# Optimization experiments

Hardware: AMD Instinct MI355X
Metric: run time of the kernel (lower is better)

Reference implementation:

```python
import jax, jax.numpy as jnp
import numpy as np

B, D, C, H = 4096, 64, 16, 512   # batch, state dim, conditional dim, MLP hidden
NBIJ, NSTEPS = 2, 8              # stacked FFJORD bijectors, fixed RK4 steps over t in [0,1]


def setup_inputs() -> dict:
    key = jax.random.key(0)
    ks = jax.random.split(key, 8)
    g = lambda k, shape, scale: (jax.random.normal(k, shape, jnp.float32) * scale).astype(jnp.float32)
    return {
        "x": jax.random.normal(ks[0], (B, D), jnp.float32),
        "cond": jax.random.normal(ks[1], (B, C), jnp.float32),
        "eps": jax.random.normal(ks[2], (NBIJ, B, D), jnp.float32),  # Hutchinson probes, one per bijector
        "W1": g(ks[3], (NBIJ, D + C + 1, H), (D + C + 1) ** -0.5),
        "b1": jnp.zeros((NBIJ, H), jnp.float32),
        "W2": g(ks[4], (NBIJ, H, H), H ** -0.5),
        "b2": jnp.zeros((NBIJ, H), jnp.float32),
        "W3": g(ks[5], (NBIJ, H, D), H ** -0.5),
        "b3": jnp.zeros((NBIJ, D), jnp.float32),
    }


def _mlp(t, y, cond, W1, b1, W2, b2, W3, b3):
    # state_time_derivative_fn(t, x, conditional_input=cond) -> [B, D]
    tcol = jnp.full((y.shape[0], 1), t, y.dtype)
    h = jnp.tanh(jnp.concatenate([y, cond, tcol], axis=-1) @ W1 + b1)
    h = jnp.tanh(h @ W2 + b2)
    return h @ W3 + b3


def _integrate(x, cond, eps, params):
    # Augmented ODE: dy/dt = f(t,y), d(logdet)/dt = tr(df/dy) ~= eps^T J eps (Hutchinson)
    dt = jnp.float32(1.0 / NSTEPS)

    def aug(t, y):
        f = lambda z: _mlp(t, z, cond, *params)
        out, vjp_fn = jax.vjp(f, y)
        (epsJ,) = vjp_fn(eps)
        return out, jnp.sum(epsJ * eps, axis=-1)

    def step(carry, i):
        y, ld = carry
        t = i * dt
        k1, l1 = aug(t, y)
        k2, l2 = aug(t + 0.5 * dt, y + (0.5 * dt) * k1)
        k3, l3 = aug(t + 0.5 * dt, y + (0.5 * dt) * k2)
        k4, l4 = aug(t + dt, y + dt * k3)
        y = y + (dt / 6.0) * (k1 + 2.0 * k2 + 2.0 * k3 + k4)
        ld = ld + (dt / 6.0) * (l1 + 2.0 * l2 + 2.0 * l3 + l4)
        return (y, ld), None

    ld0 = jnp.zeros((x.shape[0],), x.dtype)
    (y, ld), _ = jax.lax.scan(step, (x, ld0), jnp.arange(NSTEPS, dtype=x.dtype))
    return y, ld


def reference(x, cond, eps, W1, b1, W2, b2, W3, b3):
    # Chain forward: bijector0 then bijector1 (tfb.Chain(reversed(...)) applies in build order)
    y = x
    ld = jnp.zeros((x.shape[0],), x.dtype)
    for ib in range(NBIJ):
        params = (W1[ib], b1[ib], W2[ib], b2[ib], W3[ib], b3[ib])
        y, d = _integrate(y, cond, eps[ib], params)
        ld = ld + d
    # augmented output: transformed state + accumulated log|det J|
    return jnp.concatenate([y, ld[:, None]], axis=-1)
```

## Files before the change

### kernel.cpp

```cpp
#include <hip/hip_runtime.h>


typedef __attribute__((ext_vector_type(8))) short short8;
typedef __attribute__((ext_vector_type(4))) float f32x4;
typedef __attribute__((ext_vector_type(4))) int int4v;

#define MFMA_B16(a, b, c) __builtin_amdgcn_mfma_f32_16x16x32_bf16((a), (b), (c), 0, 0, 0)
#define MFMA_I8(a, b, c)  __builtin_amdgcn_mfma_i32_16x16x64_i8((a), (b), (c), 0, 0, 0)

__device__ __forceinline__ unsigned short f2bf(float f) {
  union { float f; unsigned u; } v; v.f = f;
  return (unsigned short)((v.u + 0x7FFFu + ((v.u >> 16) & 1u)) >> 16);
}
__device__ __forceinline__ float bf2f(unsigned short u) {
  union { unsigned u; float f; } v; v.u = ((unsigned)u) << 16; return v.f;
}
__device__ __forceinline__ float fast_tanh(float x) {
  float e = __expf(2.f * x);
  return 1.f - 2.f * __builtin_amdgcn_rcpf(e + 1.f);
}


__global__ void prep_scales(const float* __restrict__ W2, float* __restrict__ sc) {
  int idx = blockIdx.x * 256 + threadIdx.x;
  if (idx >= 1024) return;
  int ib = idx >> 9, n = idx & 511;
  const float* W = W2 + (size_t)ib * 262144;
  float m = 0.f;
  for (int k = 0; k < 512; ++k) m = fmaxf(m, fabsf(W[(size_t)k * 512 + n]));
  sc[idx] = fmaxf(m, 1e-8f);
}

__global__ void prep_bf16(const float* __restrict__ W1, const float* __restrict__ W2,
                          const float* __restrict__ W3, unsigned short* __restrict__ ws) {
  int o = blockIdx.x * 256 + threadIdx.x;
  char* ws8 = (char*)ws;
  const float* sc = (const float*)(ws8 + 1114112);
  if (o < 98304) {
    int ib = o / 49152, r = o % 49152, n = r / 96, k = r % 96;
    ws[o] = (k < 81) ? f2bf(W1[(size_t)ib * 41472 + k * 512 + n]) : (unsigned short)0;
  } else if (o < 622592) {
    int b = o - 98304;
    int ib = b / 262144, b2 = b % 262144;
    int p = b2 / 32768, r2 = b2 % 32768, n = r2 / 64, kk = r2 & 63;
    int k = p * 64 + (kk ^ (((n >> 1) & 3) << 4));
    float w = W2[(size_t)ib * 262144 + (size_t)k * 512 + n];
    float s = sc[ib * 512 + n];
    int q = (int)rintf(w * (127.f / s));
    q = q > 127 ? 127 : (q < -127 ? -127 : q);
    ws8[196608 + b] = (char)q;
  } else if (o < 688128) {
    int o2 = o - 622592;
    int ib = o2 / 32768, r = o2 % 32768, n = r / 512, k = r % 512;
    ws[360448 + o2] = f2bf(W3[(size_t)ib * 32768 + k * 64 + n]);
  } else if (o < 753664) {
    int o2 = o - 688128;
    ws[425984 + o2] = f2bf(W3[o2]);
  } else if (o < 819200) {
    int o2 = o - 753664;
    int ib = o2 / 32768, r = o2 % 32768, h = r / 64, d = r % 64;
    ws[491520 + o2] = f2bf(W1[(size_t)ib * 41472 + d * 512 + h]);
  }
}

#define ZS 104
#define HS 520
#define H8 528
#define INV2 (1.f / 16129.f)

#define ISSUE_STAGE(WP, KS, BUF) do {                                                   \
    const char* _s = (WP) + (KS) * 32768 + (wave << 11) + (lane << 4);                  \
    char* _d = &Bst[(BUF)][wave << 11];                                                 \
    __builtin_amdgcn_global_load_lds(                                                   \
        (const __attribute__((address_space(1))) void*)_s,                              \
        (__attribute__((address_space(3))) void*)_d, 16, 0, 0);                         \
    __builtin_amdgcn_global_load_lds(                                                   \
        (const __attribute__((address_space(1))) void*)(_s + 1024),                     \
        (__attribute__((address_space(3))) void*)(_d + 1024), 16, 0, 0);                \
  } while (0)

__global__ __launch_bounds__(1024) void ffjord_mfma(
    const float* __restrict__ x, const float* __restrict__ cond, const float* __restrict__ eps,
    const float* __restrict__ b1g, const float* __restrict__ b2g, const float* __restrict__ b3g,
    const unsigned short* __restrict__ ws, float* __restrict__ out) {
  __shared__ unsigned short zA[16 * ZS];
  __shared__ __align__(16) char h1A8[16 * H8];
  __shared__ __align__(16) char vA8[16 * H8];
  __shared__ unsigned short h2A[16 * HS];
  __shared__ __align__(16) char Bst[3][32768];
  __shared__ float f_s[16][64];
  __shared__ float l_row[16], ld_row[16], ldacc[16];
  __shared__ int sgu[16];

  const int t = threadIdx.x;
  const int wave = t >> 6;
  const int lane = t & 63;
  const int lane15 = lane & 15;
  const int q8 = (lane >> 4) * 8;
  const int q16 = (lane >> 4) * 16;
  const int rowb = q8 >> 1;
  const int row0 = blockIdx.x * 16;
  const int ws32 = wave * 32;
  const int nt3 = wave & 3;
  const int kb3 = (wave >> 2) * 128;
  const int tm = t >> 6, td = t & 63;

  const int kk2b = q16 ^ (((lane15 >> 1) & 3) << 4);

  float ycur, ytmp, yacc = 0.f;
  {
    float xv = x[(size_t)(row0 + tm) * 64 + td];
    ycur = xv; ytmp = xv;
  }
  if (t < 512) {
    int m = t >> 5, kk = t & 31;
    zA[m * ZS + 64 + kk] = (kk < 16) ? f2bf(cond[(size_t)(row0 + m) * 16 + kk]) : (unsigned short)0;
  }
  if (t < 16) { ld_row[t] = 0.f; l_row[t] = 0.f; }

  const float dt = 0.125f;
  const float w06 = dt / 6.f, w13 = dt / 3.f;
  const char* wsb = (const char*)ws;

  for (int ib = 0; ib < 2; ++ib) {
    const unsigned short* W1f = ws + ib * 49152;
    const char* W2f8 = wsb + 196608 + ib * 262144;
    const unsigned short* W3f = ws + 360448 + ib * 32768;
    const unsigned short* W3b = ws + 425984 + ib * 32768;
    const unsigned short* W1u = ws + 491520 + ib * 32768;
    const float* scf = (const float*)(wsb + 1114112) + ib * 512;
    const float* b1b = b1g + ib * 512;
    const float* b2b = b2g + ib * 512;
    const float* b3b = b3g + ib * 64;

    zA[tm * ZS + td] = f2bf(eps[((size_t)ib * 4096 + row0 + tm) * 64 + td]);
    if (t < 16) sgu[t] = 0;
    __syncthreads();

    float e3r[8], ur[8];
    {
      f32x4 a0 = {0,0,0,0}, a1 = {0,0,0,0};
      f32x4 u0 = {0,0,0,0}, u1 = {0,0,0,0};
      const unsigned short* ap = zA + lane15 * ZS + q8;
      const unsigned short* wp3 = W3b + (size_t)(ws32 + lane15) * 64 + q8;
      const unsigned short* wpu = W1u + (size_t)(ws32 + lane15) * 64 + q8;
      #pragma unroll
      for (int kk = 0; kk < 64; kk += 32) {
        short8 a = *(const short8*)(ap + kk);
        a0 = MFMA_B16(a, *(const short8*)(wp3 + kk),           a0);
        a1 = MFMA_B16(a, *(const short8*)(wp3 + 16 * 64 + kk), a1);
        u0 = MFMA_B16(a, *(const short8*)(wpu + kk),           u0);
        u1 = MFMA_B16(a, *(const short8*)(wpu + 16 * 64 + kk), u1);
      }
      #pragma unroll
      for (int rg = 0; rg < 4; ++rg) {
        e3r[rg] = a0[rg]; e3r[4 + rg] = a1[rg];
        ur[rg] = u0[rg];  ur[4 + rg] = u1[rg];
      }
      #pragma unroll
      for (int rg = 0; rg < 4; ++rg) {
        float mr = fmaxf(fabsf(ur[rg]), fabsf(ur[4 + rg]));
        #pragma unroll
        for (int o = 1; o < 16; o <<= 1) mr = fmaxf(mr, __shfl_xor(mr, o));
        if (lane15 == 0) atomicMax(&sgu[rowb + rg], __float_as_int(mr));
      }
    }
    __syncthreads();

    float su_[4], qsv[4];
    #pragma unroll
    for (int rg = 0; rg < 4; ++rg) {
      float sg = fmaxf(__int_as_float(sgu[rowb + rg]), 1e-20f);
      su_[rg] = sg * INV2;
      qsv[rg] = 127.f / sg;
    }

    for (int it = 0; it < 32; ++it) {
      const int s = it & 3;
      const float te = (it >> 2) * dt + ((s == 0) ? 0.f : (s == 3) ? dt : 0.5f * dt);

      if (it > 0) {
        int sp = (it - 1) & 3;
        float fv = f_s[tm][td] + b3b[td];
        if (sp == 0)      { yacc = ycur + w06 * fv; ytmp = ycur + 0.5f * dt * fv; }
        else if (sp == 1) { yacc += w13 * fv;       ytmp = ycur + 0.5f * dt * fv; }
        else if (sp == 2) { yacc += w13 * fv;       ytmp = ycur + dt * fv; }
        else              { float yn = yacc + w06 * fv; ycur = yn; ytmp = yn; }
      }
      zA[tm * ZS + td] = f2bf(ytmp);
      f_s[tm][td] = 0.f;
      if (t < 16) {
        if (it > 0) {
          int sp = (it - 1) & 3;
          float lv = l_row[t];
          if (sp == 0)      ldacc[t] = w06 * lv;
          else if (sp < 3)  ldacc[t] += w13 * lv;
          else              ld_row[t] += ldacc[t] + w06 * lv;
        }
        l_row[t] = 0.f;
        zA[t * ZS + 80] = f2bf(te);
      }
      if (it == 0) { ISSUE_STAGE(W2f8, 0, 0); ISSUE_STAGE(W2f8, 1, 1); }
      __syncthreads();

      {
        f32x4 a0 = {0,0,0,0}, a1 = {0,0,0,0};
        const unsigned short* ap = zA + lane15 * ZS + q8;
        const unsigned short* wp = W1f + (size_t)(ws32 + lane15) * 96 + q8;
        #pragma unroll
        for (int k0 = 0; k0 < 96; k0 += 32) {
          short8 a = *(const short8*)(ap + k0);
          a0 = MFMA_B16(a, *(const short8*)(wp + k0),           a0);
          a1 = MFMA_B16(a, *(const short8*)(wp + 16 * 96 + k0), a1);
        }
        #pragma unroll
        for (int tl = 0; tl < 2; ++tl) {
          int n = ws32 + tl * 16 + lane15;
          float bias = b1b[n];
          f32x4 ac = tl ? a1 : a0;
          #pragma unroll
          for (int rg = 0; rg < 4; ++rg) {
            float th = fast_tanh(ac[rg] + bias);
            int off = (rowb + rg) * H8 + n;
            h1A8[off] = (char)__float2int_rn(th * 127.f);
            float v = (1.f - th * th) * ur[tl * 4 + rg];
            vA8[off] = (char)__float2int_rn(v * qsv[rg]);
          }
        }
      }
      __syncthreads();

      {
        int4v ha0 = {0,0,0,0}, ha1 = {0,0,0,0}, wa0 = {0,0,0,0}, wa1 = {0,0,0,0};
        const char* aph = h1A8 + lane15 * H8;
        const char* apv = vA8 + lane15 * H8;
        #pragma unroll
        for (int ks = 0; ks < 8; ++ks) {
          if (ks < 7) asm volatile("s_waitcnt vmcnt(2)" ::: "memory");
          else        asm volatile("s_waitcnt vmcnt(0)" ::: "memory");
          const char* bq = &Bst[ks % 3][wave << 11];
          int4v ah = *(const int4v*)(aph + ks * 64 + q16);
          int4v av = *(const int4v*)(apv + ks * 64 + q16);
          int4v b0 = *(const int4v*)(bq + lane15 * 64 + kk2b);
          int4v b1 = *(const int4v*)(bq + (16 + lane15) * 64 + kk2b);
          if (ks < 6) {
            asm volatile("s_waitcnt lgkmcnt(4)" ::: "memory");
            ISSUE_STAGE(W2f8, ks + 2, (ks + 2) % 3);
          }
          ha0 = MFMA_I8(ah, b0, ha0);
          ha1 = MFMA_I8(ah, b1, ha1);
          wa0 = MFMA_I8(av, b0, wa0);
          wa1 = MFMA_I8(av, b1, wa1);
        }
        float p0 = 0.f, p1 = 0.f, p2 = 0.f, p3 = 0.f;
        #pragma unroll
        for (int tl = 0; tl < 2; ++tl) {
          int n = ws32 + tl * 16 + lane15;
          float bias = b2b[n];
          float dq = scf[n] * INV2;
          float dqw = scf[n];
          int4v hac = tl ? ha1 : ha0;
          int4v wac = tl ? wa1 : wa0;
          #pragma unroll
          for (int rg = 0; rg < 4; ++rg) {
            float h = fast_tanh((float)hac[rg] * dq + bias);
            h2A[(rowb + rg) * HS + n] = f2bf(h);
            float g2 = e3r[tl * 4 + rg] * (1.f - h * h);
            float w = (float)wac[rg] * dqw * su_[rg];
            float pc = g2 * w;
            if (rg == 0) p0 += pc; else if (rg == 1) p1 += pc;
            else if (rg == 2) p2 += pc; else p3 += pc;
          }
        }
        #pragma unroll
        for (int o = 1; o < 16; o <<= 1) {
          p0 += __shfl_xor(p0, o); p1 += __shfl_xor(p1, o);
          p2 += __shfl_xor(p2, o); p3 += __shfl_xor(p3, o);
        }
        if (lane15 == 0) {
          atomicAdd(&l_row[rowb + 0], p0); atomicAdd(&l_row[rowb + 1], p1);
          atomicAdd(&l_row[rowb + 2], p2); atomicAdd(&l_row[rowb + 3], p3);
        }
      }
      __syncthreads();

      if (it < 31) { ISSUE_STAGE(W2f8, 0, 0); ISSUE_STAGE(W2f8, 1, 1); }
      {
        f32x4 c0 = {0,0,0,0};
        const unsigned short* ap3 = h2A + lane15 * HS + kb3 + q8;
        const unsigned short* wp3 = W3f + (size_t)(nt3 * 16 + lane15) * 512 + kb3 + q8;
        #pragma unroll
        for (int kk = 0; kk < 128; kk += 32)
          c0 = MFMA_B16(*(const short8*)(ap3 + kk), *(const short8*)(wp3 + kk), c0);
        #pragma unroll
        for (int rg = 0; rg < 4; ++rg)
          atomicAdd(&f_s[rowb + rg][nt3 * 16 + lane15], c0[rg]);
      }
      __syncthreads();
    }

    {
      float fv = f_s[tm][td] + b3b[td];
      float yn = yacc + w06 * fv;
      ycur = yn; ytmp = yn;
    }
    if (t < 16) { ld_row[t] += ldacc[t] + w06 * l_row[t]; l_row[t] = 0.f; }
    __syncthreads();
  }

  out[(size_t)(row0 + tm) * 65 + td] = ycur;
  if (t < 16) out[(size_t)(row0 + t) * 65 + 64] = ld_row[t];
}

extern "C" void kernel_launch(void* const* d_in, const int* in_sizes, int n_in,
                              void* d_out, int out_size, void* d_ws, size_t ws_size,
                              hipStream_t stream) {
  (void)in_sizes; (void)n_in; (void)out_size; (void)ws_size;
  const float* x    = (const float*)d_in[0];
  const float* cond = (const float*)d_in[1];
  const float* eps  = (const float*)d_in[2];
  const float* W1   = (const float*)d_in[3];
  const float* b1   = (const float*)d_in[4];
  const float* W2   = (const float*)d_in[5];
  const float* b2   = (const float*)d_in[6];
  const float* W3   = (const float*)d_in[7];
  const float* b3   = (const float*)d_in[8];
  float* out = (float*)d_out;
  unsigned short* ws = (unsigned short*)d_ws;

  prep_scales<<<4, 256, 0, stream>>>(W2, (float*)((char*)ws + 1114112));
  const int prep_total = 819200;
  prep_bf16<<<(prep_total + 255) / 256, 256, 0, stream>>>(W1, W2, W3, ws);
  ffjord_mfma<<<256, 1024, 0, stream>>>(x, cond, eps, b1, b2, b3, ws, out);
}
```

Before: 1.037 ms.

## Parallelize W2 scale reduction and quantize W2 via coalesced LDS transpose

Replaces the 4-block per-column max reduction with a 64-block reduction that combines partial maxima using integer atomicMax on float bits, after a zero-init kernel. W2 int8 quantization moves to its own kernel that loads 64x64 tiles coalesced into shared memory and writes packed 16-byte words, instead of one strided float load per byte. The remaining bf16 conversions stay in a smaller elementwise kernel. This is meant to cut the preprocessing cost that sits before the main kernel, at the price of two extra kernel launches.

```diff
diff --git a/kernel.cpp b/kernel.cpp
--- a/kernel.cpp
+++ b/kernel.cpp
@@ -21,45 +21,83 @@
 }
 
 
+__global__ void prep_sc_init(float* __restrict__ sc) {
+  int i = blockIdx.x * 256 + threadIdx.x;
+  if (i < 1024) ((int*)sc)[i] = 0;
+}
+
 __global__ void prep_scales(const float* __restrict__ W2, float* __restrict__ sc) {
-  int idx = blockIdx.x * 256 + threadIdx.x;
-  if (idx >= 1024) return;
-  int ib = idx >> 9, n = idx & 511;
-  const float* W = W2 + (size_t)ib * 262144;
-  float m = 0.f;
-  for (int k = 0; k < 512; ++k) m = fmaxf(m, fabsf(W[(size_t)k * 512 + n]));
-  sc[idx] = fmaxf(m, 1e-8f);
-}
-
-__global__ void prep_bf16(const float* __restrict__ W1, const float* __restrict__ W2,
-                          const float* __restrict__ W3, unsigned short* __restrict__ ws) {
+  int ib = blockIdx.x >> 5, rb = blockIdx.x & 31;
+  const float* W = W2 + (size_t)ib * 262144 + (size_t)rb * 16 * 512;
+  int c = threadIdx.x;
+  float m0 = 0.f, m1 = 0.f;
+  #pragma unroll 4
+  for (int r = 0; r < 16; ++r) {
+    m0 = fmaxf(m0, fabsf(W[r * 512 + c]));
+    m1 = fmaxf(m1, fabsf(W[r * 512 + c + 256]));
+  }
+  atomicMax((int*)sc + ib * 512 + c,       __float_as_int(m0));
+  atomicMax((int*)sc + ib * 512 + c + 256, __float_as_int(m1));
+}
+
+__global__ void prep_w2(const float* __restrict__ W2, unsigned short* __restrict__ ws) {
+  __shared__ float tile[64][65];
+  __shared__ float scl[64];
+  const int t = threadIdx.x;
+  const int blk = blockIdx.x;
+  const int ib = blk >> 6, p = (blk >> 3) & 7, nb = blk & 7;
+  const float* W = W2 + (size_t)ib * 262144 + (size_t)(p * 64) * 512 + nb * 64;
+  const int* scI = (const int*)((const char*)ws + 1114112) + ib * 512 + nb * 64;
+
+  #pragma unroll
+  for (int pass = 0; pass < 16; ++pass) {
+    int k = (t >> 6) + pass * 4, n = t & 63;
+    tile[k][n] = W[(size_t)k * 512 + n];
+  }
+  if (t < 64) scl[t] = fmaxf(__int_as_float(scI[t]), 1e-8f);
+  __syncthreads();
+
+  char* out = (char*)ws + 196608 + (size_t)ib * 262144 + (size_t)p * 32768
+            + (size_t)nb * 64 * 64;
+  const int nl = t >> 2, kk0 = (t & 3) * 16;
+  const int n = nb * 64 + nl;
+  const int sw = ((n >> 1) & 3) << 4;
+  const float inv = 127.f / scl[nl];
+  int words[4];
+  #pragma unroll
+  for (int w4 = 0; w4 < 4; ++w4) {
+    int v = 0;
+    #pragma unroll
+    for (int j = 0; j < 4; ++j) {
+      int kk = kk0 + w4 * 4 + j;
+      int kloc = kk ^ sw;
+      int q = (int)rintf(tile[kloc][nl] * inv);
+      q = q > 127 ? 127 : (q < -127 ? -127 : q);
+      v |= (q & 0xff) << (8 * j);
+    }
+    words[w4] = v;
+  }
+  int4v o4 = {words[0], words[1], words[2], words[3]};
+  *(int4v*)(out + (size_t)nl * 64 + kk0) = o4;
+}
+
+__global__ void prep_rest(const float* __restrict__ W1, const float* __restrict__ W3,
+                          unsigned short* __restrict__ ws) {
   int o = blockIdx.x * 256 + threadIdx.x;
-  char* ws8 = (char*)ws;
-  const float* sc = (const float*)(ws8 + 1114112);
   if (o < 98304) {
     int ib = o / 49152, r = o % 49152, n = r / 96, k = r % 96;
     ws[o] = (k < 81) ? f2bf(W1[(size_t)ib * 41472 + k * 512 + n]) : (unsigned short)0;
-  } else if (o < 622592) {
-    int b = o - 98304;
-    int ib = b / 262144, b2 = b % 262144;
-    int p = b2 / 32768, r2 = b2 % 32768, n = r2 / 64, kk = r2 & 63;
-    int k = p * 64 + (kk ^ (((n >> 1) & 3) << 4));
-    float w = W2[(size_t)ib * 262144 + (size_t)k * 512 + n];
-    float s = sc[ib * 512 + n];
-    int q = (int)rintf(w * (127.f / s));
-    q = q > 127 ? 127 : (q < -127 ? -127 : q);
-    ws8[196608 + b] = (char)q;
-  } else if (o < 688128) {
-    int o2 = o - 622592;
-    int ib = o2 / 32768, r = o2 % 32768, n = r / 512, k = r % 512;
+  } else if (o < 163840) {
+    int o2 = o - 98304;
+    int ib = o2 >> 15, r = o2 & 32767, n = r / 512, k = r % 512;
     ws[360448 + o2] = f2bf(W3[(size_t)ib * 32768 + k * 64 + n]);
-  } else if (o < 753664) {
-    int o2 = o - 688128;
+  } else if (o < 229376) {
+    int o2 = o - 163840;
     ws[425984 + o2] = f2bf(W3[o2]);
-  } else if (o < 819200) {
-    int o2 = o - 753664;
-    int ib = o2 / 32768, r = o2 % 32768, h = r / 64, d = r % 64;
-    ws[491520 + o2] = f2bf(W1[(size_t)ib * 41472 + d * 512 + h]);
+  } else if (o < 294912) {
+    int o2 = o - 229376;
+    int ib = o2 >> 15, r = o2 & 32767, h = r / 64, d = r & 63;
+    ws[491520 + o2] = f2bf(W1[(size_t)ib * 41472 + (size_t)d * 512 + h]);
   }
 }
 
@@ -327,9 +365,11 @@
   const float* b3   = (const float*)d_in[8];
   float* out = (float*)d_out;
   unsigned short* ws = (unsigned short*)d_ws;
-
-  prep_scales<<<4, 256, 0, stream>>>(W2, (float*)((char*)ws + 1114112));
-  const int prep_total = 819200;
-  prep_bf16<<<(prep_total + 255) / 256, 256, 0, stream>>>(W1, W2, W3, ws);
+  float* sc = (float*)((char*)ws + 1114112);
+
+  prep_sc_init<<<4, 256, 0, stream>>>(sc);
+  prep_scales<<<64, 256, 0, stream>>>(W2, sc);
+  prep_w2<<<128, 256, 0, stream>>>(W2, ws);
+  prep_rest<<<1152, 256, 0, stream>>>(W1, W3, ws);
   ffjord_mfma<<<256, 1024, 0, stream>>>(x, cond, eps, b1, b2, b3, ws, out);
 }
```

Result: faster. 962.6 us (-7.2%).
